# Kernel tuning notes

Measured on AMD Instinct MI355X. Metric: run time of the kernel, lower is better.

Reference implementation:

```python
import jax, jax.numpy as jnp
import numpy as np

H, KVH, HD, E, TOPK = 16, 4, 128, 8, 2
EPS = 1.1920929e-07  # fp32 machine eps, matches F.rms_norm default


def _rms(v):
    return v * jax.lax.rsqrt(jnp.mean(jnp.square(v), axis=-1, keepdims=True) + EPS)


def _rope(t, cos, sin):
    d = t.shape[-1] // 2
    t1, t2 = t[..., :d], t[..., d:]
    return jnp.concatenate([t1 * cos + t2 * sin, -t1 * sin + t2 * cos], axis=-1)


def setup_inputs():
    key = jax.random.key(0)
    ks = jax.random.split(key, 10)
    B, T, C, D = 2, 1024, 2048, 512
    # real rotary tables (broadcast over batch and heads)
    inv = 1.0 / (10000.0 ** (np.arange(HD // 2, dtype=np.float64) / (HD // 2)))
    ang = np.arange(T, dtype=np.float64)[:, None] * inv[None, :]
    cos = jnp.asarray(np.cos(ang), jnp.float32)[None, :, None, :]
    sin = jnp.asarray(np.sin(ang), jnp.float32)[None, :, None, :]
    w = lambda k, shp, fan: jax.random.normal(k, shp, jnp.float32) * (fan ** -0.5)
    return {
        'x': jax.random.normal(ks[0], (B, T, C), jnp.float32),
        'cos': cos, 'sin': sin,
        'Wq': w(ks[1], (C, C), C),
        'Wk': w(ks[2], (C, KVH * HD), C),
        'Wv': w(ks[3], (C, KVH * HD), C),
        'Wo': w(ks[4], (C, C), C),
        'Wr': w(ks[5], (C, E), C),
        'Ws1': w(ks[6], (C, D), C),
        'Ws2': w(ks[7], (D, C), D),
        'We1': w(ks[8], (E, C, D), C),
        'We2': w(ks[9], (E, D, C), D),
    }


def reference(x, cos, sin, Wq, Wk, Wv, Wo, Wr, Ws1, Ws2, We1, We2):
    B, T, C = x.shape
    # ---- attention (pre-norm, RoPE, QK-norm, GQA, causal SDPA) ----
    xn = _rms(x)
    q = _rms(_rope((xn @ Wq).reshape(B, T, H, HD), cos, sin))      # [B,T,H,HD]
    k = _rms(_rope((xn @ Wk).reshape(B, T, KVH, HD), cos, sin))    # [B,T,KVH,HD]
    v = (xn @ Wv).reshape(B, T, KVH, HD)
    rep = H // KVH
    k = jnp.repeat(k, rep, axis=2)
    v = jnp.repeat(v, rep, axis=2)
    scores = jnp.einsum('bthd,bshd->bhts', q, k) / np.float32(np.sqrt(HD))
    causal = jnp.tril(jnp.ones((T, T), bool))
    scores = jnp.where(causal, scores, jnp.float32(-np.inf))
    att = jax.nn.softmax(scores, axis=-1)
    y = jnp.einsum('bhts,bshd->bthd', att, v).reshape(B, T, C) @ Wo
    x = x + y
    # ---- DeepSeekMoE (shared expert + top-k routed experts) ----
    xf = _rms(x).reshape(-1, C)                                    # [N,C]
    N = xf.shape[0]
    shared = jnp.square(jax.nn.relu(xf @ Ws1)) @ Ws2               # [N,C]
    logits = xf @ Wr                                               # [N,E]
    tk_w, tk_idx = jax.lax.top_k(logits, TOPK)
    tk_w = jax.nn.softmax(tk_w.astype(jnp.float32), axis=-1).astype(x.dtype)
    # scatter top-k probs into dense per-expert gates (indices unique per row)
    gates = jnp.zeros((N, E), x.dtype).at[jnp.arange(N)[:, None], tk_idx].set(tk_w)
    h = jnp.square(jax.nn.relu(jnp.einsum('nc,ecd->end', xf, We1)))  # [E,N,D]
    routed = jnp.einsum('end,edc,ne->nc', h, We2, gates)             # [N,C]
    return x + (shared + routed).reshape(B, T, C)
```

## Files before the change

### kernel.cpp

```cpp
#include <hip/hip_runtime.h>

typedef _Float16 h16;
typedef _Float16 half8 __attribute__((ext_vector_type(8)));
typedef float f32x4 __attribute__((ext_vector_type(4)));

#define EPS_RMS 1.1920929e-07f
#define MiB (1ull << 20)

__device__ __forceinline__ void gload_lds16(const void* g, void* l) {
  __builtin_amdgcn_global_load_lds(
      (const __attribute__((address_space(1))) unsigned int*)g,
      (__attribute__((address_space(3))) unsigned int*)l, 16, 0, 0);
}

struct GemmP {
  const h16* Ah; const h16* Al;
  const h16* Bh; const h16* Bl;
  float* Cf; h16* Ch; h16* Cl;
  const float* R;
  const int* cnt; const int* off; const int* perm;
  long sAz, sBz, sCzHi, sCzLo;
  int M, N, K, lda, ldb, ldc;
  int zAoff, zBoff, zCoff, bzShift, czHiShift, czLoMask;
  float outScale;
};

template <int SPLIT, int EPI, int USECNT, int GATHER, int ASYNC>
__global__ __launch_bounds__(256, 4) void gemm_k(GemmP p) {
  constexpr int NP = SPLIT ? 2 : 1;
  constexpr int NBUF = (ASYNC == 1) ? 2 : 1;
  constexpr int APAD = (ASYNC == 1) ? 32 : 40;
  constexpr int BPAD = (ASYNC >= 1) ? 32 : 40;
  __shared__ __align__(16) h16 As[NBUF][NP][128][APAD];
  __shared__ __align__(16) h16 Bs[NBUF][NP][128][BPAD];
  __shared__ int permLds[GATHER ? 128 : 1];

  const int nwg = gridDim.x * gridDim.y;
  const int flat = blockIdx.y * gridDim.x + blockIdx.x;
  const int q8 = nwg >> 3, r8 = nwg & 7;
  const int xcd = flat & 7, sub = flat >> 3;
  const int swz = (xcd < r8 ? xcd * (q8 + 1) : r8 * (q8 + 1) + (xcd - r8) * q8) + sub;
  const int bm = swz % gridDim.x, bn = swz / gridDim.x;
  const int zl = blockIdx.z;

  int Meff, rowbase;
  if (USECNT) {
    Meff = p.cnt[zl]; rowbase = p.off[zl];
    if (bm * 128 >= Meff) return;
  } else { Meff = p.M; rowbase = 0; }

  const int zA = zl + p.zAoff, zB = zl + p.zBoff, zC = zl + p.zCoff;
  const h16* Ah = p.Ah + (size_t)zA * p.sAz;
  const h16* Al = SPLIT ? p.Al + (size_t)zA * p.sAz : (const h16*)0;
  const size_t bofs = (size_t)(zB >> p.bzShift) * p.sBz;
  const h16* Bh = p.Bh + bofs;
  const h16* Bl = SPLIT ? p.Bl + bofs : (const h16*)0;
  const size_t cofs = (size_t)(zC >> p.czHiShift) * p.sCzHi +
                      (size_t)(zC & p.czLoMask) * p.sCzLo;

  const int tid = threadIdx.x;
  const int lane = tid & 63;
  const int wid = tid >> 6, wr = wid >> 1, wc = wid & 1;
  const int fr = lane & 15, fq = lane >> 4;

  if (GATHER) {
    if (tid < 128) {
      const int local = bm * 128 + tid;
      permLds[tid] = (local < Meff) ? p.perm[rowbase + local] : -1;
    }
    __syncthreads();
  }

  const long arow0 = (long)rowbase + (long)bm * 128;

  const f32x4 fz = {0.f, 0.f, 0.f, 0.f};
  f32x4 acc[4][4];
#pragma unroll
  for (int m = 0; m < 4; ++m)
#pragma unroll
    for (int n = 0; n < 4; ++n) acc[m][n] = fz;

  const int nkt = p.K / 32;

  auto compute = [&](int buf) {
    half8 af[NP][4], bf[NP][4];
#pragma unroll
    for (int m = 0; m < 4; ++m) {
      const int r = wr * 64 + m * 16 + fr;
      af[0][m] = *(const half8*)&As[buf][0][r][fq * 8];
      if (SPLIT) af[1][m] = *(const half8*)&As[buf][1][r][fq * 8];
    }
#pragma unroll
    for (int n = 0; n < 4; ++n) {
      const int c = wc * 64 + n * 16 + fr;
      bf[0][n] = *(const half8*)&Bs[buf][0][c][fq * 8];
      if (SPLIT) bf[1][n] = *(const half8*)&Bs[buf][1][c][fq * 8];
    }
#pragma unroll
    for (int m = 0; m < 4; ++m)
#pragma unroll
      for (int n = 0; n < 4; ++n) {
        acc[m][n] = __builtin_amdgcn_mfma_f32_16x16x32_f16(af[0][m], bf[0][n], acc[m][n], 0, 0, 0);
        if (SPLIT) {
          acc[m][n] = __builtin_amdgcn_mfma_f32_16x16x32_f16(af[0][m], bf[1][n], acc[m][n], 0, 0, 0);
          acc[m][n] = __builtin_amdgcn_mfma_f32_16x16x32_f16(af[1][m], bf[0][n], acc[m][n], 0, 0, 0);
        }
      }
  };

  if constexpr (ASYNC == 1) {
    auto stage = [&](int buf, int kt) {
      const int kb = kt * 32;
#pragma unroll
      for (int it = 0; it < 2; ++it) {
        const int d = (tid + it * 256) * 16;
        const int row = d >> 6;
        const int oct = (d >> 4) & 3;
        const size_t gb = ((size_t)(bn * 128 + row)) * p.ldb + kb + oct * 8;
        gload_lds16(Bh + gb, (char*)&Bs[buf][0][0][0] + d);
        if (SPLIT) gload_lds16(Bl + gb, (char*)&Bs[buf][1][0][0] + d);
        const size_t ga = (size_t)(arow0 + row) * p.lda + kb + oct * 8;
        gload_lds16(Ah + ga, (char*)&As[buf][0][0][0] + d);
        if (SPLIT) gload_lds16(Al + ga, (char*)&As[buf][1][0][0] + d);
      }
    };
    stage(0, 0);
    __syncthreads();
    int cur = 0;
    for (int kt = 0; kt < nkt; ++kt) {
      if (kt + 1 < nkt) stage(cur ^ 1, kt + 1);
      compute(cur);
      __syncthreads();
      cur ^= 1;
    }
  } else {
    for (int kt = 0; kt < nkt; ++kt) {
      if (kt) __syncthreads();
      const int kb = kt * 32;
      if constexpr (ASYNC == 2) {
#pragma unroll
        for (int it = 0; it < 2; ++it) {
          const int d = (tid + it * 256) * 16;
          const int row = d >> 6;
          const int oct = (d >> 4) & 3;
          const size_t gb = ((size_t)(bn * 128 + row)) * p.ldb + kb + oct * 8;
          gload_lds16(Bh + gb, (char*)&Bs[0][0][0][0] + d);
          if (SPLIT) gload_lds16(Bl + gb, (char*)&Bs[0][1][0][0] + d);
        }
      }
#pragma unroll
      for (int s = 0; s < 2; ++s) {
        const int seg = tid * 2 + s;
        const int row = seg >> 2, ks = (seg & 3) * 8;
        const int local = bm * 128 + row;
        bool av; long arow;
        if (GATHER) { const int tk2 = permLds[row]; av = (tk2 >= 0); arow = tk2; }
        else { av = (local < Meff); arow = (long)rowbase + local; }
        half8 vh = {0,0,0,0,0,0,0,0}, vl = {0,0,0,0,0,0,0,0};
        if (av) {
          vh = *(const half8*)(Ah + arow * (size_t)p.lda + kb + ks);
          if (SPLIT) vl = *(const half8*)(Al + arow * (size_t)p.lda + kb + ks);
        }
        *(half8*)&As[0][0][row][ks] = vh;
        if (SPLIT) *(half8*)&As[0][1][row][ks] = vl;
        if constexpr (ASYNC == 0) {
          const long brow = (long)bn * 128 + row;
          *(half8*)&Bs[0][0][row][ks] = *(const half8*)(Bh + brow * (size_t)p.ldb + kb + ks);
          if (SPLIT)
            *(half8*)&Bs[0][1][row][ks] = *(const half8*)(Bl + brow * (size_t)p.ldb + kb + ks);
        }
      }
      __syncthreads();
      compute(0);
    }
  }

#pragma unroll
  for (int m = 0; m < 4; ++m)
#pragma unroll
    for (int n = 0; n < 4; ++n)
#pragma unroll
      for (int j = 0; j < 4; ++j) {
        const int rl = wr * 64 + m * 16 + fq * 4 + j;
        const int cl = wc * 64 + n * 16 + fr;
        const int local = bm * 128 + rl;
        if (local >= Meff) continue;
        const size_t idx = cofs + ((size_t)rowbase + local) * p.ldc + (size_t)bn * 128 + cl;
        const float v = acc[m][n][j] * p.outScale;
        if (EPI == 0) p.Cf[idx] = v;
        else if (EPI == 1) p.Cf[idx] = v + p.R[idx];
        else if (EPI == 2) {
          const h16 hh = (h16)v;
          p.Ch[idx] = hh; p.Cl[idx] = (h16)(v - (float)hh);
        } else if (EPI == 3) {
          const float r2 = v > 0.f ? v * v : 0.f;
          p.Ch[idx] = (h16)r2;
        } else {
          p.Ch[idx] = (h16)v;
        }
      }
}

__global__ __launch_bounds__(512, 4) void flash_k(
    const h16* __restrict__ Qh, const h16* __restrict__ Ql,
    const h16* __restrict__ Kh, const h16* __restrict__ Kl,
    const h16* __restrict__ Vh, const h16* __restrict__ Vl,
    h16* __restrict__ yh, h16* __restrict__ yl,
    float* __restrict__ yp, float* __restrict__ mp, float* __restrict__ lp) {
  __shared__ __align__(16) h16 Ks[2][32][136];
  __shared__ __align__(16) h16 Vs[2][128][40];
  __shared__ __align__(16) h16 Ps[8][2][16][40];

  const int QBT[12]  = {3, 7, 7, 6, 6, 2, 5, 5, 4, 4, 1, 0};
  const int CHT[12]  = {0, 0, 1, 0, 1, 0, 0, 1, 0, 1, 0, 0};
  const int FULT[12] = {1, 0, 0, 0, 0, 1, 0, 0, 0, 0, 1, 1};

  const int z = blockIdx.x, item = blockIdx.y;
  const int qb = QBT[item], chunk = CHT[item], full = FULT[item];
  const int nt = (qb + 1) * 4;
  const int tBeg = full ? 0 : (chunk ? nt / 2 : 0);
  const int tEnd = full ? nt : (chunk ? nt : nt / 2);

  const int b = z >> 4, h = z & 15;
  const size_t qoff = (size_t)z * 131072;
  const size_t koff = (size_t)(b * 4 + (h >> 2)) * 131072;

  const int tid = threadIdx.x;
  const int lane = tid & 63, w = tid >> 6;
  const int fr = lane & 15, fq = lane >> 4;

  const int qrow = qb * 128 + w * 16 + fr;
  half8 qa[2][4];
#pragma unroll
  for (int kt = 0; kt < 4; ++kt) {
    qa[0][kt] = *(const half8*)(Qh + qoff + (size_t)qrow * 128 + kt * 32 + fq * 8);
    qa[1][kt] = *(const half8*)(Ql + qoff + (size_t)qrow * 128 + kt * 32 + fq * 8);
  }

  const int kRow = tid >> 4, kSeg = tid & 15;
  const int vRow = tid >> 2, vSeg = tid & 3;

  half8 kreg[2], vreg[2];
  auto loadKV = [&](int t) {
    const int kvb = t * 32;
#pragma unroll
    for (int pl = 0; pl < 2; ++pl) {
      const h16* kp = pl ? Kl : Kh;
      const h16* vp = pl ? Vl : Vh;
      kreg[pl] = *(const half8*)(kp + koff + (size_t)(kvb + kRow) * 128 + kSeg * 8);
      vreg[pl] = *(const half8*)(vp + koff + (size_t)vRow * 1024 + kvb + vSeg * 8);
    }
  };

  const f32x4 fz = {0.f, 0.f, 0.f, 0.f};
  f32x4 y[8];
#pragma unroll
  for (int n = 0; n < 8; ++n) y[n] = fz;
  float mrow[4] = {-3.0e38f, -3.0e38f, -3.0e38f, -3.0e38f};
  float lrow[4] = {0.f, 0.f, 0.f, 0.f};

  loadKV(tBeg);
  for (int t = tBeg; t < tEnd; ++t) {
    const int kvb = t * 32;
    if (t != tBeg) __syncthreads();
#pragma unroll
    for (int pl = 0; pl < 2; ++pl) {
      *(half8*)&Ks[pl][kRow][kSeg * 8] = kreg[pl];
      *(half8*)&Vs[pl][vRow][vSeg * 8] = vreg[pl];
    }
    __syncthreads();
    if (t + 1 < tEnd) loadKV(t + 1);

    f32x4 sf[2] = {fz, fz};
#pragma unroll
    for (int n = 0; n < 2; ++n)
#pragma unroll
      for (int kt = 0; kt < 4; ++kt) {
        const half8 bh2 = *(const half8*)&Ks[0][n * 16 + fr][kt * 32 + fq * 8];
        const half8 bl2 = *(const half8*)&Ks[1][n * 16 + fr][kt * 32 + fq * 8];
        sf[n] = __builtin_amdgcn_mfma_f32_16x16x32_f16(qa[0][kt], bh2, sf[n], 0, 0, 0);
        sf[n] = __builtin_amdgcn_mfma_f32_16x16x32_f16(qa[0][kt], bl2, sf[n], 0, 0, 0);
        sf[n] = __builtin_amdgcn_mfma_f32_16x16x32_f16(qa[1][kt], bh2, sf[n], 0, 0, 0);
      }

    if (kvb + 31 > qb * 128) {
#pragma unroll
      for (int n = 0; n < 2; ++n)
#pragma unroll
        for (int j = 0; j < 4; ++j) {
          const int kvg = kvb + n * 16 + fr;
          const int qg = qb * 128 + w * 16 + fq * 4 + j;
          if (kvg > qg) sf[n][j] = -3.0e38f;
        }
    }

    float al[4];
#pragma unroll
    for (int j = 0; j < 4; ++j) {
      float tm = fmaxf(sf[0][j], sf[1][j]);
#pragma unroll
      for (int msk = 1; msk < 16; msk <<= 1) tm = fmaxf(tm, __shfl_xor(tm, msk, 16));
      const float mn = fmaxf(mrow[j], tm);
      al[j] = __expf(mrow[j] - mn);
      mrow[j] = mn;
      sf[0][j] = __expf(sf[0][j] - mn);
      sf[1][j] = __expf(sf[1][j] - mn);
      float ts = sf[0][j] + sf[1][j];
#pragma unroll
      for (int msk = 1; msk < 16; msk <<= 1) ts += __shfl_xor(ts, msk, 16);
      lrow[j] = lrow[j] * al[j] + ts;
    }
#pragma unroll
    for (int n = 0; n < 8; ++n)
#pragma unroll
      for (int j = 0; j < 4; ++j) y[n][j] *= al[j];

#pragma unroll
    for (int n = 0; n < 2; ++n)
#pragma unroll
      for (int j = 0; j < 4; ++j) {
        const float pp = sf[n][j] * 1024.f;
        const h16 hh = (h16)pp;
        Ps[w][0][fq * 4 + j][n * 16 + fr] = hh;
        Ps[w][1][fq * 4 + j][n * 16 + fr] = (h16)(pp - (float)hh);
      }

    const half8 pah = *(const half8*)&Ps[w][0][fr][fq * 8];
    const half8 pal = *(const half8*)&Ps[w][1][fr][fq * 8];
#pragma unroll
    for (int n = 0; n < 8; ++n) {
      const half8 vh2 = *(const half8*)&Vs[0][n * 16 + fr][fq * 8];
      const half8 vl2 = *(const half8*)&Vs[1][n * 16 + fr][fq * 8];
      y[n] = __builtin_amdgcn_mfma_f32_16x16x32_f16(pah, vh2, y[n], 0, 0, 0);
      y[n] = __builtin_amdgcn_mfma_f32_16x16x32_f16(pah, vl2, y[n], 0, 0, 0);
      y[n] = __builtin_amdgcn_mfma_f32_16x16x32_f16(pal, vh2, y[n], 0, 0, 0);
    }
  }

  if (full) {
#pragma unroll
    for (int n = 0; n < 8; ++n)
#pragma unroll
      for (int j = 0; j < 4; ++j) {
        const int row = qb * 128 + w * 16 + fq * 4 + j;
        const int col = h * 128 + n * 16 + fr;
        const float v = y[n][j] / (1024.f * lrow[j]);
        const size_t idx = ((size_t)(b * 1024 + row)) * 2048 + col;
        const h16 hh = (h16)v;
        yh[idx] = hh; yl[idx] = (h16)(v - (float)hh);
      }
  } else {
#pragma unroll
    for (int j = 0; j < 4; ++j) {
      const int qrl = w * 16 + fq * 4 + j;
      const int q512 = (qb - 4) * 128 + qrl;
      const size_t rbase = (((size_t)chunk * 32 + z) * 512 + q512);
#pragma unroll
      for (int n = 0; n < 8; ++n)
        yp[rbase * 128 + n * 16 + fr] = y[n][j];
      if (fr == 0) { mp[rbase] = mrow[j]; lp[rbase] = lrow[j]; }
    }
  }
}

__global__ void comb_k(const float* __restrict__ yp, const float* __restrict__ mp,
                       const float* __restrict__ lp,
                       h16* __restrict__ yh, h16* __restrict__ yl) {
  const int qh = blockIdx.x, z = blockIdx.y;
  const int b = z >> 4, h = z & 15;
  const int tid = threadIdx.x;
  for (int idx = tid; idx < 16384; idx += 256) {
    const int r = idx >> 7, d = idx & 127;
    const int q512 = qh * 128 + r;
    const size_t r0 = ((size_t)0 * 32 + z) * 512 + q512;
    const size_t r1 = ((size_t)1 * 32 + z) * 512 + q512;
    const float m1 = mp[r0], m2 = mp[r1];
    const float l1 = lp[r0], l2 = lp[r1];
    const float M = fmaxf(m1, m2);
    const float e1 = __expf(m1 - M), e2 = __expf(m2 - M);
    const float inv = 1.f / (1024.f * (l1 * e1 + l2 * e2));
    const float v = (yp[r0 * 128 + d] * e1 + yp[r1 * 128 + d] * e2) * inv;
    const size_t o = ((size_t)(b * 1024 + (4 + qh) * 128 + r)) * 2048 + h * 128 + d;
    const h16 hh = (h16)v;
    yh[o] = hh; yl[o] = (h16)(v - (float)hh);
  }
}

__global__ void tsplit_k(const float* __restrict__ W, h16* __restrict__ Th,
                         h16* __restrict__ Tl, int K, int N, float scale, int wantLo) {
  const size_t eoff = (size_t)blockIdx.z * (size_t)K * N;
  W += eoff; Th += eoff; if (Tl) Tl += eoff;
  __shared__ float tile[32][33];
  const int nt = blockIdx.x * 32, kt = blockIdx.y * 32;
  const int c = threadIdx.x & 31, r0 = threadIdx.x >> 5;
#pragma unroll
  for (int rr = 0; rr < 4; ++rr)
    tile[r0 + rr * 8][c] = W[(size_t)(kt + r0 + rr * 8) * N + nt + c];
  __syncthreads();
  const int t = threadIdx.x;
  const int pl = t >> 7;
  if (pl == 1 && !wantLo) return;
  const int n = (t & 127) >> 2, ks = (t & 3) * 8;
  half8 o;
#pragma unroll
  for (int i = 0; i < 8; ++i) {
    const float v = tile[ks + i][n] * scale;
    const h16 hh = (h16)v;
    o[i] = pl ? (h16)(v - (float)hh) : hh;
  }
  h16* dst = pl ? Tl : Th;
  *(half8*)&dst[(size_t)(nt + n) * K + kt + ks] = o;
}

template <int WLO>
__global__ void rms_k(const float* __restrict__ X, h16* __restrict__ H,
                      h16* __restrict__ L) {
  const int row = blockIdx.x;
  const float* x = X + (size_t)row * 2048;
  __shared__ float red[256];
  const int tid = threadIdx.x;
  float ss = 0.f;
  for (int c = tid; c < 2048; c += 256) { const float v = x[c]; ss += v * v; }
  red[tid] = ss; __syncthreads();
  for (int t = 128; t > 0; t >>= 1) {
    if (tid < t) red[tid] += red[tid + t];
    __syncthreads();
  }
  const float sc = rsqrtf(red[0] * (1.f / 2048.f) + EPS_RMS);
  for (int c = tid; c < 2048; c += 256) {
    const float v = x[c] * sc;
    const size_t o2 = (size_t)row * 2048 + c;
    const h16 hh = (h16)v;
    H[o2] = hh;
    if (WLO) L[o2] = (h16)(v - (float)hh);
  }
}

__global__ void rmsrouter_k(const float* __restrict__ x2, const float* __restrict__ Wr,
                            h16* __restrict__ xfh,
                            int* __restrict__ idx2, float* __restrict__ g2,
                            int* __restrict__ cnt) {
  const int n = blockIdx.x, tid = threadIdx.x;
  __shared__ float redss[256];
  __shared__ float red8[256][8];
  const float* xr = x2 + (size_t)n * 2048;
  float ss = 0.f;
  float part[8] = {0, 0, 0, 0, 0, 0, 0, 0};
  for (int c = tid; c < 2048; c += 256) {
    const float v = xr[c];
    ss += v * v;
    const float* w2 = Wr + (size_t)c * 8;
#pragma unroll
    for (int e = 0; e < 8; ++e) part[e] += v * w2[e];
  }
  redss[tid] = ss;
#pragma unroll
  for (int e = 0; e < 8; ++e) red8[tid][e] = part[e];
  __syncthreads();
  for (int t = 128; t > 0; t >>= 1) {
    if (tid < t) {
      redss[tid] += redss[tid + t];
#pragma unroll
      for (int e = 0; e < 8; ++e) red8[tid][e] += red8[tid + t][e];
    }
    __syncthreads();
  }
  const float sc = rsqrtf(redss[0] * (1.f / 2048.f) + EPS_RMS);
  for (int c = tid; c < 2048; c += 256)
    xfh[(size_t)n * 2048 + c] = (h16)(xr[c] * sc);
  if (tid == 0) {
    float l[8];
#pragma unroll
    for (int e = 0; e < 8; ++e) l[e] = red8[0][e] * sc;
    int i1 = 0;
    for (int e = 1; e < 8; ++e) if (l[e] > l[i1]) i1 = e;
    int i2 = (i1 == 0) ? 1 : 0;
    for (int e = 0; e < 8; ++e) if (e != i1 && l[e] > l[i2]) i2 = e;
    const float e2 = __expf(l[i2] - l[i1]);
    const float inv = 1.f / (1.f + e2);
    idx2[n * 2] = i1; idx2[n * 2 + 1] = i2;
    g2[n * 2] = inv; g2[n * 2 + 1] = e2 * inv;
    atomicAdd(&cnt[i1], 1); atomicAdd(&cnt[i2], 1);
  }
}

__global__ void rope_k(const float* __restrict__ qkv, const float* __restrict__ cosT,
                       const float* __restrict__ sinT,
                       h16* __restrict__ Qh, h16* __restrict__ Ql,
                       h16* __restrict__ Kh, h16* __restrict__ Kl,
                       h16* __restrict__ Vh, h16* __restrict__ Vl) {
  const int tok = blockIdx.x;
  const int b = tok >> 10, t = tok & 1023;
  const int u = blockIdx.y, d = threadIdx.x;
  __shared__ float buf[128];
  __shared__ float red[128];
  int col;
  if (u < 16) col = u * 128 + d;
  else if (u < 20) col = 2048 + (u - 16) * 128 + d;
  else col = 2560 + (u - 20) * 128 + d;
  float v = qkv[(size_t)tok * 3072 + col];
  if (u < 20) {
    buf[d] = v; __syncthreads();
    float r;
    if (d < 64) {
      const float c = cosT[t * 64 + d], s = sinT[t * 64 + d];
      r = buf[d] * c + buf[d + 64] * s;
    } else {
      const float c = cosT[t * 64 + d - 64], s = sinT[t * 64 + d - 64];
      r = -buf[d - 64] * s + buf[d] * c;
    }
    red[d] = r * r; __syncthreads();
    for (int tt = 64; tt > 0; tt >>= 1) {
      if (d < tt) red[d] += red[d + tt];
      __syncthreads();
    }
    v = r * rsqrtf(red[0] * (1.f / 128.f) + EPS_RMS);
    if (u < 16) v *= 0.08838834764831845f;
  }
  const h16 hh = (h16)v;
  const h16 lo = (h16)(v - (float)hh);
  if (u < 16) {
    const size_t o2 = (((size_t)(b * 16 + u)) * 1024 + t) * 128 + d;
    Qh[o2] = hh; Ql[o2] = lo;
  } else if (u < 20) {
    const size_t o2 = (((size_t)(b * 4 + (u - 16))) * 1024 + t) * 128 + d;
    Kh[o2] = hh; Kl[o2] = lo;
  } else {
    const size_t o2 = ((size_t)(b * 4 + (u - 20))) * 131072 + (size_t)d * 1024 + t;
    Vh[o2] = hh; Vl[o2] = lo;
  }
}

__global__ void zero8_k(int* __restrict__ p) {
  if (threadIdx.x < 16 && blockIdx.x == 0) p[threadIdx.x] = 0;
}

__global__ void scan_k(int* __restrict__ cnt, int* __restrict__ off,
                       int* __restrict__ base) {
  if (threadIdx.x == 0 && blockIdx.x == 0) {
    int a = 0;
    for (int e = 0; e < 8; ++e) { off[e] = a; base[e] = a; a += cnt[e]; }
    off[8] = a; base[8] = a; cnt[8] = 2048;
  }
}

__global__ void assign_k(const int* __restrict__ idx2, int* __restrict__ base,
                         int* __restrict__ perm, int* __restrict__ pos2) {
  const int n = blockIdx.x * 256 + threadIdx.x;
  if (n >= 2048) return;
  perm[4096 + n] = n;
  for (int j = 0; j < 2; ++j) {
    const int e = idx2[n * 2 + j];
    const int pos = atomicAdd(&base[e], 1);
    perm[pos] = n;
    pos2[n * 2 + j] = pos;
  }
}

__global__ void combine_k(const float* __restrict__ x2, const h16* __restrict__ rpx,
                          const int* __restrict__ pos2,
                          const float* __restrict__ g2, float* __restrict__ out) {
  const int n = blockIdx.x;
  const int p0 = pos2[n * 2], p1 = pos2[n * 2 + 1];
  const float g0 = g2[n * 2], g1 = g2[n * 2 + 1];
  const h16* sh = rpx + (size_t)(4096 + n) * 2048;
  for (int c = threadIdx.x; c < 2048; c += 256) {
    const size_t i = (size_t)n * 2048 + c;
    out[i] = x2[i] + (float)sh[c] + g0 * (float)rpx[(size_t)p0 * 2048 + c]
             + g1 * (float)rpx[(size_t)p1 * 2048 + c];
  }
}

extern "C" void kernel_launch(void* const* d_in, const int* in_sizes, int n_in,
                              void* d_out, int out_size, void* d_ws, size_t ws_size,
                              hipStream_t stream) {
  const float* x    = (const float*)d_in[0];
  const float* cosT = (const float*)d_in[1];
  const float* sinT = (const float*)d_in[2];
  const float* Wq   = (const float*)d_in[3];
  const float* Wk   = (const float*)d_in[4];
  const float* Wv   = (const float*)d_in[5];
  const float* Wo   = (const float*)d_in[6];
  const float* Wr   = (const float*)d_in[7];
  const float* Ws1  = (const float*)d_in[8];
  const float* Ws2  = (const float*)d_in[9];
  const float* We1  = (const float*)d_in[10];
  const float* We2  = (const float*)d_in[11];
  float* out = (float*)d_out;

  unsigned char* W = (unsigned char*)d_ws;
  int*   idx2 = (int*)(W + 0);
  float* g2   = (float*)(W + 16 * 1024);
  int*   cnt  = (int*)(W + 32 * 1024);
  int*   offs = (int*)(W + 33 * 1024);
  int*   base = (int*)(W + 34 * 1024);
  int*   pos2 = (int*)(W + 36 * 1024);
  int*   perm = (int*)(W + 56 * 1024);
  h16* W1h = (h16*)(W + 1 * MiB);
  h16* W1l = (h16*)(W + 13 * MiB);
  h16* W2h = (h16*)(W + 1 * MiB);
  h16* W2l = (h16*)(W + 9 * MiB);
  h16* xnh = (h16*)(W + 25 * MiB);
  h16* xnl = (h16*)(W + 33 * MiB);
  h16* yh  = (h16*)(W + 25 * MiB);
  h16* yl  = (h16*)(W + 33 * MiB);
  h16* xfh = (h16*)(W + 25 * MiB);
  float* qkv = (float*)(W + 41 * MiB);
  float* ypart = (float*)(W + 41 * MiB);
  float* mpart = (float*)(W + 57 * MiB);
  float* lpart = (float*)(W + 58 * MiB);
  h16* hcomb = (h16*)(W + 41 * MiB);
  h16* Qh = (h16*)(W + 65 * MiB);
  h16* Ql = (h16*)(W + 73 * MiB);
  h16* Kh = (h16*)(W + 81 * MiB);
  h16* Kl = (h16*)(W + 83 * MiB);
  h16* Vh = (h16*)(W + 85 * MiB);
  h16* Vl = (h16*)(W + 87 * MiB);
  h16* rpx = (h16*)(W + 65 * MiB);
  float* x2 = (float*)(W + 89 * MiB);
  h16* WeT = (h16*)(W + 105 * MiB);
  h16* WsPlane8 = WeT + (size_t)8 * 1048576;

  const float WS = 64.f;
  const float IWS = 1.f / 64.f;

  tsplit_k<<<dim3(64, 64, 1), 256, 0, stream>>>(Wq, W1h, W1l, 2048, 2048, WS, 1);
  tsplit_k<<<dim3(16, 64, 1), 256, 0, stream>>>(Wk, W1h + (size_t)2048 * 2048,
                                                W1l + (size_t)2048 * 2048, 2048, 512, WS, 1);
  tsplit_k<<<dim3(16, 64, 1), 256, 0, stream>>>(Wv, W1h + (size_t)2560 * 2048,
                                                W1l + (size_t)2560 * 2048, 2048, 512, WS, 1);
  zero8_k<<<1, 64, 0, stream>>>(cnt);
  rms_k<1><<<2048, 256, 0, stream>>>(x, xnh, xnl);
  {
    GemmP p{};
    p.Ah = xnh; p.Al = xnl; p.Bh = W1h; p.Bl = W1l; p.Cf = qkv;
    p.M = 2048; p.N = 3072; p.K = 2048; p.lda = 2048; p.ldb = 2048; p.ldc = 3072;
    p.outScale = IWS;
    gemm_k<1, 0, 0, 0, 1><<<dim3(16, 24, 1), 256, 0, stream>>>(p);
  }

  rope_k<<<dim3(2048, 24, 1), 128, 0, stream>>>(qkv, cosT, sinT, Qh, Ql, Kh, Kl, Vh, Vl);

  tsplit_k<<<dim3(64, 64, 1), 256, 0, stream>>>(Wo, W2h, W2l, 2048, 2048, WS, 1);
  flash_k<<<dim3(32, 12, 1), 512, 0, stream>>>(Qh, Ql, Kh, Kl, Vh, Vl, yh, yl,
                                               ypart, mpart, lpart);
  comb_k<<<dim3(4, 32, 1), 256, 0, stream>>>(ypart, mpart, lpart, yh, yl);

  {
    GemmP p{};
    p.Ah = yh; p.Al = yl; p.Bh = W2h; p.Bl = W2l; p.Cf = x2; p.R = x;
    p.M = 2048; p.N = 2048; p.K = 2048; p.lda = 2048; p.ldb = 2048; p.ldc = 2048;
    p.outScale = IWS;
    gemm_k<1, 1, 0, 0, 1><<<dim3(16, 16, 1), 256, 0, stream>>>(p);
  }

  rmsrouter_k<<<2048, 256, 0, stream>>>(x2, Wr, xfh, idx2, g2, cnt);
  scan_k<<<1, 64, 0, stream>>>(cnt, offs, base);
  assign_k<<<8, 256, 0, stream>>>(idx2, base, perm, pos2);

  tsplit_k<<<dim3(16, 64, 8), 256, 0, stream>>>(We1, WeT, (h16*)0, 2048, 512, WS, 0);
  tsplit_k<<<dim3(16, 64, 1), 256, 0, stream>>>(Ws1, WsPlane8, (h16*)0, 2048, 512, WS, 0);
  {
    GemmP p{};
    p.Ah = xfh; p.Bh = WeT; p.Ch = hcomb;
    p.N = 512; p.K = 2048; p.lda = 2048; p.ldb = 2048; p.ldc = 512;
    p.sBz = (long)512 * 2048; p.bzShift = 0;
    p.cnt = cnt; p.off = offs; p.perm = perm;
    p.outScale = IWS;
    gemm_k<0, 3, 1, 1, 2><<<dim3(16, 4, 9), 256, 0, stream>>>(p);
  }
  tsplit_k<<<dim3(64, 16, 8), 256, 0, stream>>>(We2, WeT, (h16*)0, 512, 2048, WS, 0);
  tsplit_k<<<dim3(64, 16, 1), 256, 0, stream>>>(Ws2, WsPlane8, (h16*)0, 512, 2048, WS, 0);
  {
    GemmP p{};
    p.Ah = hcomb; p.Bh = WeT; p.Ch = rpx;
    p.N = 2048; p.K = 512; p.lda = 512; p.ldb = 512; p.ldc = 2048;
    p.sBz = (long)2048 * 512; p.bzShift = 0;
    p.cnt = cnt; p.off = offs; p.perm = perm;
    p.outScale = IWS;
    gemm_k<0, 4, 1, 0, 1><<<dim3(16, 16, 9), 256, 0, stream>>>(p);
  }

  combine_k<<<2048, 256, 0, stream>>>(x2, rpx, pos2, g2, out);
}
```

Before: 541.1 us.

## Split-K the Wo GEMM and fold the residual add into the router; double-buffer gathered GEMM

The Wo projection GEMM is now split along K into two halves over blockIdx.z, each writing a partial fp32 output. The RMS/router kernel sums x plus both partials, writes x2 and proceeds as before, so the residual epilogue is dropped. This raises occupancy on the 256-block Wo GEMM at the cost of extra partial-buffer traffic. Separately, the ASYNC==2 path (the gathered expert-1 GEMM) becomes double-buffered, prefetching A into registers and B into LDS one k-step ahead.

```diff
diff --git a/kernel.cpp b/kernel.cpp
--- a/kernel.cpp
+++ b/kernel.cpp
@@ -25,10 +25,10 @@
   float outScale;
 };
 
-template <int SPLIT, int EPI, int USECNT, int GATHER, int ASYNC>
+template <int SPLIT, int EPI, int USECNT, int GATHER, int ASYNC, int KS>
 __global__ __launch_bounds__(256, 4) void gemm_k(GemmP p) {
   constexpr int NP = SPLIT ? 2 : 1;
-  constexpr int NBUF = (ASYNC == 1) ? 2 : 1;
+  constexpr int NBUF = (ASYNC >= 1) ? 2 : 1;
   constexpr int APAD = (ASYNC == 1) ? 32 : 40;
   constexpr int BPAD = (ASYNC >= 1) ? 32 : 40;
   __shared__ __align__(16) h16 As[NBUF][NP][128][APAD];
@@ -81,6 +81,8 @@
     for (int n = 0; n < 4; ++n) acc[m][n] = fz;
 
   const int nkt = p.K / 32;
+  const int ktBeg = (KS > 1) ? zl * (nkt / KS) : 0;
+  const int ktEnd = (KS > 1) ? ktBeg + nkt / KS : nkt;
 
   auto compute = [&](int buf) {
     half8 af[NP][4], bf[NP][4];
@@ -124,30 +126,60 @@
         if (SPLIT) gload_lds16(Al + ga, (char*)&As[buf][1][0][0] + d);
       }
     };
-    stage(0, 0);
+    stage(0, ktBeg);
     __syncthreads();
     int cur = 0;
-    for (int kt = 0; kt < nkt; ++kt) {
-      if (kt + 1 < nkt) stage(cur ^ 1, kt + 1);
+    for (int kt = ktBeg; kt < ktEnd; ++kt) {
+      if (kt + 1 < ktEnd) stage(cur ^ 1, kt + 1);
       compute(cur);
       __syncthreads();
       cur ^= 1;
     }
+  } else if constexpr (ASYNC == 2) {
+    half8 aPre[2];
+    auto loadA = [&](int kt) {
+#pragma unroll
+      for (int s = 0; s < 2; ++s) {
+        const int seg = tid * 2 + s;
+        const int row = seg >> 2, ks = (seg & 3) * 8;
+        bool av; long arow;
+        if (GATHER) { const int tk2 = permLds[row]; av = (tk2 >= 0); arow = tk2; }
+        else { const int local = bm * 128 + row; av = (local < Meff); arow = (long)rowbase + local; }
+        half8 v = {0,0,0,0,0,0,0,0};
+        if (av) v = *(const half8*)(Ah + arow * (size_t)p.lda + kt * 32 + ks);
+        aPre[s] = v;
+      }
+    };
+    auto stageB2 = [&](int buf, int kt) {
+      const int kb = kt * 32;
+#pragma unroll
+      for (int it = 0; it < 2; ++it) {
+        const int d = (tid + it * 256) * 16;
+        const int row = d >> 6;
+        const int oct = (d >> 4) & 3;
+        const size_t gb = ((size_t)(bn * 128 + row)) * p.ldb + kb + oct * 8;
+        gload_lds16(Bh + gb, (char*)&Bs[buf][0][0][0] + d);
+      }
+    };
+    loadA(ktBeg);
+    stageB2(0, ktBeg);
+    int cur = 0;
+    for (int kt = ktBeg; kt < ktEnd; ++kt) {
+#pragma unroll
+      for (int s = 0; s < 2; ++s) {
+        const int seg = tid * 2 + s;
+        const int row = seg >> 2, ks = (seg & 3) * 8;
+        *(half8*)&As[cur][0][row][ks] = aPre[s];
+      }
+      __syncthreads();
+      if (kt + 1 < ktEnd) { loadA(kt + 1); stageB2(cur ^ 1, kt + 1); }
+      compute(cur);
+      cur ^= 1;
+    }
   } else {
-    for (int kt = 0; kt < nkt; ++kt) {
-      if (kt) __syncthreads();
+    for (int kt = ktBeg; kt < ktEnd; ++kt) {
+      if (kt != ktBeg) __syncthreads();
       const int kb = kt * 32;
-      if constexpr (ASYNC == 2) {
-#pragma unroll
-        for (int it = 0; it < 2; ++it) {
-          const int d = (tid + it * 256) * 16;
-          const int row = d >> 6;
-          const int oct = (d >> 4) & 3;
-          const size_t gb = ((size_t)(bn * 128 + row)) * p.ldb + kb + oct * 8;
-          gload_lds16(Bh + gb, (char*)&Bs[0][0][0][0] + d);
-          if (SPLIT) gload_lds16(Bl + gb, (char*)&Bs[0][1][0][0] + d);
-        }
-      }
 #pragma unroll
       for (int s = 0; s < 2; ++s) {
         const int seg = tid * 2 + s;
@@ -163,12 +195,10 @@
         }
         *(half8*)&As[0][0][row][ks] = vh;
         if (SPLIT) *(half8*)&As[0][1][row][ks] = vl;
-        if constexpr (ASYNC == 0) {
-          const long brow = (long)bn * 128 + row;
-          *(half8*)&Bs[0][0][row][ks] = *(const half8*)(Bh + brow * (size_t)p.ldb + kb + ks);
-          if (SPLIT)
-            *(half8*)&Bs[0][1][row][ks] = *(const half8*)(Bl + brow * (size_t)p.ldb + kb + ks);
-        }
+        const long brow = (long)bn * 128 + row;
+        *(half8*)&Bs[0][0][row][ks] = *(const half8*)(Bh + brow * (size_t)p.ldb + kb + ks);
+        if (SPLIT)
+          *(half8*)&Bs[0][1][row][ks] = *(const half8*)(Bl + brow * (size_t)p.ldb + kb + ks);
       }
       __syncthreads();
       compute(0);
@@ -436,18 +466,24 @@
   }
 }
 
-__global__ void rmsrouter_k(const float* __restrict__ x2, const float* __restrict__ Wr,
-                            h16* __restrict__ xfh,
+__global__ void rmsrouter_k(const float* __restrict__ x, const float* __restrict__ P0,
+                            const float* __restrict__ P1, const float* __restrict__ Wr,
+                            float* __restrict__ x2, h16* __restrict__ xfh,
                             int* __restrict__ idx2, float* __restrict__ g2,
                             int* __restrict__ cnt) {
   const int n = blockIdx.x, tid = threadIdx.x;
   __shared__ float redss[256];
   __shared__ float red8[256][8];
-  const float* xr = x2 + (size_t)n * 2048;
+  const size_t rb = (size_t)n * 2048;
+  float vreg[8];
   float ss = 0.f;
   float part[8] = {0, 0, 0, 0, 0, 0, 0, 0};
-  for (int c = tid; c < 2048; c += 256) {
-    const float v = xr[c];
+#pragma unroll
+  for (int i = 0; i < 8; ++i) {
+    const int c = tid + i * 256;
+    const float v = x[rb + c] + P0[rb + c] + P1[rb + c];
+    vreg[i] = v;
+    x2[rb + c] = v;
     ss += v * v;
     const float* w2 = Wr + (size_t)c * 8;
 #pragma unroll
@@ -466,8 +502,9 @@
     __syncthreads();
   }
   const float sc = rsqrtf(redss[0] * (1.f / 2048.f) + EPS_RMS);
-  for (int c = tid; c < 2048; c += 256)
-    xfh[(size_t)n * 2048 + c] = (h16)(xr[c] * sc);
+#pragma unroll
+  for (int i = 0; i < 8; ++i)
+    xfh[rb + tid + i * 256] = (h16)(vreg[i] * sc);
   if (tid == 0) {
     float l[8];
 #pragma unroll
@@ -609,6 +646,7 @@
   float* ypart = (float*)(W + 41 * MiB);
   float* mpart = (float*)(W + 57 * MiB);
   float* lpart = (float*)(W + 58 * MiB);
+  float* wopart = (float*)(W + 41 * MiB);
   h16* hcomb = (h16*)(W + 41 * MiB);
   h16* Qh = (h16*)(W + 65 * MiB);
   h16* Ql = (h16*)(W + 73 * MiB);
@@ -636,7 +674,7 @@
     p.Ah = xnh; p.Al = xnl; p.Bh = W1h; p.Bl = W1l; p.Cf = qkv;
     p.M = 2048; p.N = 3072; p.K = 2048; p.lda = 2048; p.ldb = 2048; p.ldc = 3072;
     p.outScale = IWS;
-    gemm_k<1, 0, 0, 0, 1><<<dim3(16, 24, 1), 256, 0, stream>>>(p);
+    gemm_k<1, 0, 0, 0, 1, 1><<<dim3(16, 24, 1), 256, 0, stream>>>(p);
   }
 
   rope_k<<<dim3(2048, 24, 1), 128, 0, stream>>>(qkv, cosT, sinT, Qh, Ql, Kh, Kl, Vh, Vl);
@@ -648,13 +686,15 @@
 
   {
     GemmP p{};
-    p.Ah = yh; p.Al = yl; p.Bh = W2h; p.Bl = W2l; p.Cf = x2; p.R = x;
+    p.Ah = yh; p.Al = yl; p.Bh = W2h; p.Bl = W2l; p.Cf = wopart;
     p.M = 2048; p.N = 2048; p.K = 2048; p.lda = 2048; p.ldb = 2048; p.ldc = 2048;
+    p.sCzHi = (long)2048 * 2048;
     p.outScale = IWS;
-    gemm_k<1, 1, 0, 0, 1><<<dim3(16, 16, 1), 256, 0, stream>>>(p);
-  }
-
-  rmsrouter_k<<<2048, 256, 0, stream>>>(x2, Wr, xfh, idx2, g2, cnt);
+    gemm_k<1, 0, 0, 0, 1, 2><<<dim3(16, 16, 2), 256, 0, stream>>>(p);
+  }
+
+  rmsrouter_k<<<2048, 256, 0, stream>>>(x, wopart, wopart + (size_t)2048 * 2048,
+                                        Wr, x2, xfh, idx2, g2, cnt);
   scan_k<<<1, 64, 0, stream>>>(cnt, offs, base);
   assign_k<<<8, 256, 0, stream>>>(idx2, base, perm, pos2);
 
@@ -667,7 +707,7 @@
     p.sBz = (long)512 * 2048; p.bzShift = 0;
     p.cnt = cnt; p.off = offs; p.perm = perm;
     p.outScale = IWS;
-    gemm_k<0, 3, 1, 1, 2><<<dim3(16, 4, 9), 256, 0, stream>>>(p);
+    gemm_k<0, 3, 1, 1, 2, 1><<<dim3(16, 4, 9), 256, 0, stream>>>(p);
   }
   tsplit_k<<<dim3(64, 16, 8), 256, 0, stream>>>(We2, WeT, (h16*)0, 512, 2048, WS, 0);
   tsplit_k<<<dim3(64, 16, 1), 256, 0, stream>>>(Ws2, WsPlane8, (h16*)0, 512, 2048, WS, 0);
@@ -678,7 +718,7 @@
     p.sBz = (long)2048 * 512; p.bzShift = 0;
     p.cnt = cnt; p.off = offs; p.perm = perm;
     p.outScale = IWS;
-    gemm_k<0, 4, 1, 0, 1><<<dim3(16, 16, 9), 256, 0, stream>>>(p);
+    gemm_k<0, 4, 1, 0, 1, 1><<<dim3(16, 16, 9), 256, 0, stream>>>(p);
   }
 
   combine_k<<<2048, 256, 0, stream>>>(x2, rpx, pos2, g2, out);
```

Result: faster. 500.3 us (-7.5%).
